# Kernel tuning notes

Measured on AMD Instinct MI355X. Metric: run time of the kernel, lower is better.

The kernel has to match this reference:

```python
import jax, jax.numpy as jnp
import numpy as np

KS = 3  # kernel_size
N, C_IN, C_OUT, H, W = 8, 64, 128, 256, 256


def _grid_sample_bilinear(img, gx, gy):
    """img [C,H,W]; gx, gy [Ho,Wo] normalized coords; align_corners=False, zero padding."""
    C, H_, W_ = img.shape
    ix = ((gx + 1.0) * W_ - 1.0) / 2.0
    iy = ((gy + 1.0) * H_ - 1.0) / 2.0
    x0 = jnp.floor(ix); y0 = jnp.floor(iy)
    x1 = x0 + 1.0;      y1 = y0 + 1.0
    wx1 = ix - x0; wx0 = 1.0 - wx1
    wy1 = iy - y0; wy0 = 1.0 - wy1

    def gather(yi, xi):
        valid = (xi >= 0) & (xi < W_) & (yi >= 0) & (yi < H_)
        xc = jnp.clip(xi, 0, W_ - 1).astype(jnp.int32)
        yc = jnp.clip(yi, 0, H_ - 1).astype(jnp.int32)
        v = img[:, yc, xc]  # [C,Ho,Wo]
        return v * valid[None].astype(img.dtype)

    out = (gather(y0, x0) * (wy0 * wx0)[None]
         + gather(y0, x1) * (wy0 * wx1)[None]
         + gather(y1, x0) * (wy1 * wx0)[None]
         + gather(y1, x1) * (wy1 * wx1)[None])
    return out


def setup_inputs() -> dict:
    key = jax.random.key(0)
    k1, k2, k3 = jax.random.split(key, 3)
    x = jax.random.normal(k1, (N, C_IN, H, W), dtype=jnp.float32)
    # offset conv: Conv2d(inc, 2*ks, ks, padding=(ks-1)//2, bias=False)
    offset_w = jax.random.normal(k2, (2 * KS, C_IN, KS, KS), dtype=jnp.float32) * 0.05
    # conv_kernel: Conv2d(inc, outc, kernel=(ks,1), stride=(ks,1), bias=False), kaiming fan_out
    fan_out = C_OUT * KS * 1
    conv_w = jax.random.normal(k3, (C_OUT, C_IN, KS, 1), dtype=jnp.float32) * np.sqrt(2.0 / fan_out)
    return {"x": x, "offset_w": offset_w, "conv_w": conv_w}


def reference(x, offset_w, conv_w):
    n, c, h, w = x.shape
    ks = KS
    pad = (ks - 1) // 2
    dn = ('NCHW', 'OIHW', 'NCHW')

    off = jax.lax.conv_general_dilated(x, offset_w, (1, 1), ((pad, pad), (pad, pad)),
                                       dimension_numbers=dn)  # [n,2ks,h,w]
    off = jnp.tanh(off).reshape(n, 2, ks, h, w)
    offset_y = off[:, 0]  # [n,ks,h,w]; x offsets are computed but unused in the original

    yc = (ks - 1) // 2
    # cumulative offsets radiating outward from the center row
    upper = jnp.cumsum(offset_y[:, yc:], axis=1)                       # indices yc..ks-1
    lower = jnp.cumsum(offset_y[:, :yc + 1][:, ::-1], axis=1)[:, ::-1]  # indices 0..yc
    y_new = jnp.concatenate([lower[:, :yc], upper], axis=1)            # [n,ks,h,w]

    # base grid replicates torch's repeat-then-reshape layout exactly:
    # flat pattern [-1,0,1,-1,0,1,...] of length ks*h*w, reshaped to (ks,h,w)
    vals = jnp.arange(-(ks - 1) // 2, (ks - 1) // 2 + 1, dtype=x.dtype)
    base = vals[jnp.arange(ks * h * w) % ks].reshape(ks, h, w)

    grid_y = (base[None] + y_new).reshape(n, ks * h, w)
    gy = grid_y / ((h - 1.0) / 2.0) - 1.0
    gx = jnp.full_like(gy, -1.0)  # grid_x is zeros -> 0/((w-1)/2) - 1 = -1

    sampled = jax.vmap(_grid_sample_bilinear)(x, gx, gy)  # [n,c,ks*h,w]

    out = jax.lax.conv_general_dilated(sampled, conv_w, (ks, 1), ((0, 0), (0, 0)),
                                       dimension_numbers=dn)  # [n,outc,h,w]
    return out
```

## Files before the change

kernel.cpp:

```cpp
#include <hip/hip_runtime.h>
#include <math.h>

#define H 256
#define W 256
#define NB 8
#define CIN 64
#define COUT 128
#define HW (H * W)

typedef float f4v __attribute__((ext_vector_type(4)));

__global__ __launch_bounds__(256) void kfused(const float* __restrict__ x,
                                              const float* __restrict__ offw,
                                              const float* __restrict__ convw,
                                              float* __restrict__ ynew,
                                              float* __restrict__ P) {
    if (blockIdx.z == NB) {
        __shared__ float xl[CIN * 4];
        __shared__ float wl[16 * 192];
        const int n = blockIdx.y;
        const int co0 = blockIdx.x * 16;
        const int tid = threadIdx.x;
        {
            int ci = tid >> 2, y = tid & 3;
            xl[tid] = x[(((size_t)n * CIN + ci) * H + y) * W];
        }
        for (int p = tid; p < 16 * 192; p += 256) wl[p] = convw[co0 * 192 + p];
        __syncthreads();
        if (tid < 192) {
            int co = tid / 12, t = tid - co * 12;
            int r = t >> 2, y = t & 3;
            float s = 0.f;
#pragma unroll
            for (int ci = 0; ci < CIN; ++ci) s += wl[co * 192 + ci * 3 + r] * xl[ci * 4 + y];
            P[((size_t)n * COUT + co0 + co) * 16 + t] = s;
        }
        return;
    }

    const int n = blockIdx.z;
    const int i0 = blockIdx.y * 32;
    const int j0 = blockIdx.x * 32;
    const int tid = threadIdx.x;
    const int wv = tid >> 6;
    const int lane = tid & 63;
    const int rloc = lane >> 3;
    const int q = lane & 7;
    const int orow = i0 + 8 * wv + rloc;
    const int jq = j0 + q * 4;
    const int lprev = (lane - 1) & 63;
    const int lnext = (lane + 1) & 63;

    const bool isq0 = (q == 0), isq7 = (q == 7);
    const int ecol = isq0 ? (j0 - 1) : (j0 + 32);
    const bool ecv = (isq0 | isq7) && ((unsigned)ecol < (unsigned)W);
    const int ecc = ecol < 0 ? 0 : (ecol > W - 1 ? W - 1 : ecol);

    const bool rv0 = (orow >= 1);
    const bool rv2 = (orow <= H - 2);
    const size_t ro0 = (size_t)(rv0 ? orow - 1 : 0) * W;
    const size_t ro1 = (size_t)orow * W;
    const size_t ro2 = (size_t)(rv2 ? orow + 1 : H - 1) * W;
    const bool ev0 = rv0 && ecv, ev1 = ecv, ev2 = rv2 && ecv;

    const float* xn = x + (size_t)n * CIN * HW;
    const float4 zf4 = make_float4(0.f, 0.f, 0.f, 0.f);

    float acc[3][4];
#pragma unroll
    for (int k = 0; k < 3; ++k)
#pragma unroll
        for (int d = 0; d < 4; ++d) acc[k][d] = 0.f;

#define LOADCH(c, M0, M1, M2, E0, E1, E2)                          \
    {                                                              \
        const float* xc = xn + (size_t)(c) * HW;                   \
        M0 = rv0 ? *(const float4*)(xc + ro0 + jq) : zf4;          \
        M1 = *(const float4*)(xc + ro1 + jq);                      \
        M2 = rv2 ? *(const float4*)(xc + ro2 + jq) : zf4;          \
        E0 = ev0 ? xc[ro0 + ecc] : 0.f;                            \
        E1 = ev1 ? xc[ro1 + ecc] : 0.f;                            \
        E2 = ev2 ? xc[ro2 + ecc] : 0.f;                            \
    }

#define CU(u, M, E)                                                \
    {                                                              \
        float lf = __shfl(M.w, lprev);                             \
        float rt = __shfl(M.x, lnext);                             \
        if (isq0) lf = E;                                          \
        if (isq7) rt = E;                                          \
        const float r0 = lf, r1 = M.x, r2 = M.y, r3 = M.z,         \
                    r4 = M.w, r5 = rt;                             \
        _Pragma("unroll") for (int k = 0; k < 3; ++k) {            \
            const float w0 = wp[k * 576 + (u)*3 + 0];              \
            const float w1 = wp[k * 576 + (u)*3 + 1];              \
            const float w2 = wp[k * 576 + (u)*3 + 2];              \
            acc[k][0] += r0 * w0 + r1 * w1 + r2 * w2;              \
            acc[k][1] += r1 * w0 + r2 * w1 + r3 * w2;              \
            acc[k][2] += r2 * w0 + r3 * w1 + r4 * w2;              \
            acc[k][3] += r3 * w0 + r4 * w1 + r5 * w2;              \
        }                                                          \
    }

#define COMPUTE(c, M0, M1, M2, E0, E1, E2)                         \
    {                                                              \
        const float* wp = offw + (size_t)(c) * 9;                  \
        CU(0, M0, E0) CU(1, M1, E1) CU(2, M2, E2)                  \
    }

    float4 Am0, Am1, Am2, Bm0, Bm1, Bm2;
    float Ae0, Ae1, Ae2, Be0, Be1, Be2;
    LOADCH(0, Am0, Am1, Am2, Ae0, Ae1, Ae2);
    LOADCH(1, Bm0, Bm1, Bm2, Be0, Be1, Be2);

    for (int c = 0; c < CIN; c += 2) {
        COMPUTE(c, Am0, Am1, Am2, Ae0, Ae1, Ae2);
        if (c + 2 < CIN) LOADCH(c + 2, Am0, Am1, Am2, Ae0, Ae1, Ae2);
        COMPUTE(c + 1, Bm0, Bm1, Bm2, Be0, Be1, Be2);
        if (c + 3 < CIN) LOADCH(c + 3, Bm0, Bm1, Bm2, Be0, Be1, Be2);
    }
#undef LOADCH
#undef CU
#undef COMPUTE

    float y[3][4];
#pragma unroll
    for (int d = 0; d < 4; ++d) {
        float t0 = tanhf(acc[0][d]);
        float t1 = tanhf(acc[1][d]);
        float t2 = tanhf(acc[2][d]);
        y[0][d] = t0 + t1;
        y[1][d] = t1;
        y[2][d] = t1 + t2;
    }
    size_t base = (size_t)n * 3 * HW + (size_t)orow * W + jq;
#pragma unroll
    for (int k = 0; k < 3; ++k)
        *(float4*)(ynew + base + (size_t)k * HW) =
            make_float4(y[k][0], y[k][1], y[k][2], y[k][3]);
}

__global__ __launch_bounds__(256) void kout(const float* __restrict__ ynew,
                                            const float* __restrict__ P,
                                            float* __restrict__ out) {
    __shared__ float Cs[12 * 256];
    __shared__ float Pl[128 * 16];
    const int n = blockIdx.y;
    const int i = blockIdx.x;
    const int tid = threadIdx.x;

    {
        const f4v* src = (const f4v*)(P + (size_t)n * COUT * 16);
        f4v* dst = (f4v*)Pl;
        dst[tid] = src[tid];
        dst[tid + 256] = src[tid + 256];
    }

    {
        const int j = tid;
        float c[12];
#pragma unroll
        for (int t = 0; t < 12; ++t) c[t] = 0.f;
#pragma unroll
        for (int r = 0; r < 3; ++r) {
            int rowi = 3 * i + r;
            int k = rowi >> 8;
            int i2 = rowi & 255;
            float g = (float)(((k + i2 + j) % 3) - 1) +
                      ynew[((size_t)n * 3 + k) * (H * W) + i2 * W + j];
            float gy = g / 127.5f - 1.0f;
            float iy = ((gy + 1.0f) * 256.0f - 1.0f) * 0.5f;
            float fy = floorf(iy);
            int y0 = (int)fy;
            float w1 = iy - fy;
            if ((unsigned)y0 < 4u) c[r * 4 + y0] += 0.5f * (1.0f - w1);
            int y1 = y0 + 1;
            if ((unsigned)y1 < 4u) c[r * 4 + y1] += 0.5f * w1;
        }
#pragma unroll
        for (int t = 0; t < 12; ++t) Cs[t * 256 + j] = c[t];
    }
    __syncthreads();

    const int jq = (tid & 63) * 4;
    const int cg = tid >> 6;
    float4 cc[12];
#pragma unroll
    for (int t = 0; t < 12; ++t) cc[t] = *(const float4*)&Cs[t * 256 + jq];

    float* op = out + (((size_t)n * COUT) * H + i) * W;
    for (int co = cg * 32; co < cg * 32 + 32; ++co) {
        const float4* pp = (const float4*)&Pl[co * 16];
        float4 P0 = pp[0], P1 = pp[1], P2 = pp[2];
        float pv[12] = {P0.x, P0.y, P0.z, P0.w, P1.x, P1.y, P1.z, P1.w,
                        P2.x, P2.y, P2.z, P2.w};
        f4v a = {0.f, 0.f, 0.f, 0.f};
#pragma unroll
        for (int t = 0; t < 12; ++t) {
            a.x += pv[t] * cc[t].x;
            a.y += pv[t] * cc[t].y;
            a.z += pv[t] * cc[t].z;
            a.w += pv[t] * cc[t].w;
        }
        __builtin_nontemporal_store(a, (f4v*)(op + (size_t)co * (H * W) + jq));
    }
}

extern "C" void kernel_launch(void* const* d_in, const int* in_sizes, int n_in,
                              void* d_out, int out_size, void* d_ws, size_t ws_size,
                              hipStream_t stream) {
    const float* x = (const float*)d_in[0];
    const float* offw = (const float*)d_in[1];
    const float* convw = (const float*)d_in[2];
    float* out = (float*)d_out;

    float* ynew = (float*)d_ws;
    float* P = ynew + (size_t)NB * 3 * HW;

    kfused<<<dim3(8, 8, NB + 1), 256, 0, stream>>>(x, offw, convw, ynew, P);
    kout<<<dim3(H, NB), 256, 0, stream>>>(ynew, P, out);
}
```

Before: 422.1 us.

## Split offset-conv channels across waves with per-wave LDS tiles and register rows

```diff
diff --git a/kernel.cpp b/kernel.cpp
--- a/kernel.cpp
+++ b/kernel.cpp
@@ -7,17 +7,23 @@
 #define CIN 64
 #define COUT 128
 #define HW (H * W)
+#define TROWS 34
+#define TCOLS 40
+#define TFLOATS (TROWS * TCOLS)
+#define TF4 (TFLOATS / 4)
 
 typedef float f4v __attribute__((ext_vector_type(4)));
 
-__global__ __launch_bounds__(256) void kfused(const float* __restrict__ x,
-                                              const float* __restrict__ offw,
-                                              const float* __restrict__ convw,
-                                              float* __restrict__ ynew,
-                                              float* __restrict__ P) {
+__global__ __launch_bounds__(256, 2) void kfused(const float* __restrict__ x,
+                                                 const float* __restrict__ offw,
+                                                 const float* __restrict__ convw,
+                                                 float* __restrict__ ynew,
+                                                 float* __restrict__ P) {
+    __shared__ float smem[12288];
+
     if (blockIdx.z == NB) {
-        __shared__ float xl[CIN * 4];
-        __shared__ float wl[16 * 192];
+        float* xl = smem;
+        float* wl = smem + 256;
         const int n = blockIdx.y;
         const int co0 = blockIdx.x * 16;
         const int tid = threadIdx.x;
@@ -44,100 +50,129 @@
     const int tid = threadIdx.x;
     const int wv = tid >> 6;
     const int lane = tid & 63;
-    const int rloc = lane >> 3;
+    const int rg = lane >> 3;
     const int q = lane & 7;
-    const int orow = i0 + 8 * wv + rloc;
-    const int jq = j0 + q * 4;
-    const int lprev = (lane - 1) & 63;
-    const int lnext = (lane + 1) & 63;
-
-    const bool isq0 = (q == 0), isq7 = (q == 7);
-    const int ecol = isq0 ? (j0 - 1) : (j0 + 32);
-    const bool ecv = (isq0 | isq7) && ((unsigned)ecol < (unsigned)W);
-    const int ecc = ecol < 0 ? 0 : (ecol > W - 1 ? W - 1 : ecol);
-
-    const bool rv0 = (orow >= 1);
-    const bool rv2 = (orow <= H - 2);
-    const size_t ro0 = (size_t)(rv0 ? orow - 1 : 0) * W;
-    const size_t ro1 = (size_t)orow * W;
-    const size_t ro2 = (size_t)(rv2 ? orow + 1 : H - 1) * W;
-    const bool ev0 = rv0 && ecv, ev1 = ecv, ev2 = rv2 && ecv;
-
-    const float* xn = x + (size_t)n * CIN * HW;
+
+    float* t0 = smem + wv * (2 * TFLOATS);
+    float* t1 = t0 + TFLOATS;
+
+    int offs[6];
+    bool vms[6];
+#pragma unroll
+    for (int m = 0; m < 6; ++m) {
+        int s = lane + (m << 6);
+        int a = s / 10, c4 = s - a * 10;
+        int gi = i0 - 1 + a;
+        int gj = j0 - 4 + (c4 << 2);
+        bool v = (s < TF4) && ((unsigned)gi < (unsigned)H) && ((unsigned)gj < (unsigned)W);
+        vms[m] = v;
+        offs[m] = v ? (gi * W + gj) : 0;
+    }
+
     const float4 zf4 = make_float4(0.f, 0.f, 0.f, 0.f);
-
-    float acc[3][4];
-#pragma unroll
-    for (int k = 0; k < 3; ++k)
-#pragma unroll
-        for (int d = 0; d < 4; ++d) acc[k][d] = 0.f;
-
-#define LOADCH(c, M0, M1, M2, E0, E1, E2)                          \
-    {                                                              \
-        const float* xc = xn + (size_t)(c) * HW;                   \
-        M0 = rv0 ? *(const float4*)(xc + ro0 + jq) : zf4;          \
-        M1 = *(const float4*)(xc + ro1 + jq);                      \
-        M2 = rv2 ? *(const float4*)(xc + ro2 + jq) : zf4;          \
-        E0 = ev0 ? xc[ro0 + ecc] : 0.f;                            \
-        E1 = ev1 ? xc[ro1 + ecc] : 0.f;                            \
-        E2 = ev2 ? xc[ro2 + ecc] : 0.f;                            \
-    }
-
-#define CU(u, M, E)                                                \
-    {                                                              \
-        float lf = __shfl(M.w, lprev);                             \
-        float rt = __shfl(M.x, lnext);                             \
-        if (isq0) lf = E;                                          \
-        if (isq7) rt = E;                                          \
-        const float r0 = lf, r1 = M.x, r2 = M.y, r3 = M.z,         \
-                    r4 = M.w, r5 = rt;                             \
-        _Pragma("unroll") for (int k = 0; k < 3; ++k) {            \
-            const float w0 = wp[k * 576 + (u)*3 + 0];              \
-            const float w1 = wp[k * 576 + (u)*3 + 1];              \
-            const float w2 = wp[k * 576 + (u)*3 + 2];              \
-            acc[k][0] += r0 * w0 + r1 * w1 + r2 * w2;              \
-            acc[k][1] += r1 * w0 + r2 * w1 + r3 * w2;              \
-            acc[k][2] += r2 * w0 + r3 * w1 + r4 * w2;              \
-            acc[k][3] += r3 * w0 + r4 * w1 + r5 * w2;              \
-        }                                                          \
-    }
-
-#define COMPUTE(c, M0, M1, M2, E0, E1, E2)                         \
-    {                                                              \
-        const float* wp = offw + (size_t)(c) * 9;                  \
-        CU(0, M0, E0) CU(1, M1, E1) CU(2, M2, E2)                  \
-    }
-
-    float4 Am0, Am1, Am2, Bm0, Bm1, Bm2;
-    float Ae0, Ae1, Ae2, Be0, Be1, Be2;
-    LOADCH(0, Am0, Am1, Am2, Ae0, Ae1, Ae2);
-    LOADCH(1, Bm0, Bm1, Bm2, Be0, Be1, Be2);
-
-    for (int c = 0; c < CIN; c += 2) {
-        COMPUTE(c, Am0, Am1, Am2, Ae0, Ae1, Ae2);
-        if (c + 2 < CIN) LOADCH(c + 2, Am0, Am1, Am2, Ae0, Ae1, Ae2);
-        COMPUTE(c + 1, Bm0, Bm1, Bm2, Be0, Be1, Be2);
-        if (c + 3 < CIN) LOADCH(c + 3, Bm0, Bm1, Bm2, Be0, Be1, Be2);
-    }
-#undef LOADCH
-#undef CU
-#undef COMPUTE
-
-    float y[3][4];
+    float acc[4][3][4];
+#pragma unroll
+    for (int ri = 0; ri < 4; ++ri)
+#pragma unroll
+        for (int k = 0; k < 3; ++k)
+#pragma unroll
+            for (int d = 0; d < 4; ++d) acc[ri][k][d] = 0.f;
+
+#define LOADC(cptr, R)                                                      \
+    _Pragma("unroll") for (int m = 0; m < 6; ++m)                           \
+        R[m] = vms[m] ? *(const float4*)((cptr) + offs[m]) : zf4;
+
+#define STAGE(buf, R)                                                       \
+    _Pragma("unroll") for (int m = 0; m < 6; ++m)                           \
+        if (m < 5 || lane < (TF4 - 320))                                    \
+            *(float4*)((buf) + ((lane + (m << 6)) << 2)) = R[m];
+
+#define COMPCH(buf, wp)                                                     \
+    {                                                                       \
+        _Pragma("unroll") for (int t = 0; t < 6; ++t) {                     \
+            const float* rp = (buf) + (4 * rg + t) * TCOLS + 4 * q;         \
+            float4 b0 = *(const float4*)(rp);                               \
+            float4 b1 = *(const float4*)(rp + 4);                           \
+            float4 b2 = *(const float4*)(rp + 8);                           \
+            const float r0 = b0.w, r1 = b1.x, r2 = b1.y, r3 = b1.z,         \
+                        r4 = b1.w, r5 = b2.x;                               \
+            _Pragma("unroll") for (int ri = 0; ri < 4; ++ri) {              \
+                if (ri < ((t - 2 > 0) ? t - 2 : 0) || ri > ((t < 3) ? t : 3)) continue; \
+                const int u = t - ri;                                       \
+                _Pragma("unroll") for (int k = 0; k < 3; ++k) {             \
+                    const float w0 = (wp)[k * 576 + u * 3 + 0];             \
+                    const float w1 = (wp)[k * 576 + u * 3 + 1];             \
+                    const float w2 = (wp)[k * 576 + u * 3 + 2];             \
+                    acc[ri][k][0] += r0 * w0 + r1 * w1 + r2 * w2;           \
+                    acc[ri][k][1] += r1 * w0 + r2 * w1 + r3 * w2;           \
+                    acc[ri][k][2] += r2 * w0 + r3 * w1 + r4 * w2;           \
+                    acc[ri][k][3] += r3 * w0 + r4 * w1 + r5 * w2;           \
+                }                                                           \
+            }                                                               \
+        }                                                                   \
+    }
+
+    const int c0 = wv << 4;
+    const float* xw = x + ((size_t)n * CIN + c0) * HW;
+    const float* wp0 = offw + (size_t)c0 * 9;
+
+    float4 RA[6], RB[6];
+    LOADC(xw, RA);
+    LOADC(xw + HW, RB);
+
+    for (int cc = 0; cc < 16; cc += 2) {
+        STAGE(t0, RA);
+        if (cc + 2 < 16) {
+            const float* xp = xw + (size_t)(cc + 2) * HW;
+            LOADC(xp, RA);
+        }
+        COMPCH(t0, wp0 + (size_t)cc * 9);
+        STAGE(t1, RB);
+        if (cc + 3 < 16) {
+            const float* xp = xw + (size_t)(cc + 3) * HW;
+            LOADC(xp, RB);
+        }
+        COMPCH(t1, wp0 + (size_t)(cc + 1) * 9);
+    }
+#undef LOADC
+#undef STAGE
+#undef COMPCH
+
+    __syncthreads();
+#pragma unroll
+    for (int ri = 0; ri < 4; ++ri)
+#pragma unroll
+        for (int k = 0; k < 3; ++k)
+#pragma unroll
+            for (int d = 0; d < 4; ++d)
+                smem[((wv * 48 + ri * 12 + k * 4 + d) << 6) + lane] = acc[ri][k][d];
+    __syncthreads();
+
+    const int row = tid >> 3;
+    const int q2 = tid & 7;
+    const int srcl = ((row >> 2) << 3) | q2;
+    const int rbase = (row & 3) * 12;
+
+    float y0[4], y1[4], y2[4];
 #pragma unroll
     for (int d = 0; d < 4; ++d) {
-        float t0 = tanhf(acc[0][d]);
-        float t1 = tanhf(acc[1][d]);
-        float t2 = tanhf(acc[2][d]);
-        y[0][d] = t0 + t1;
-        y[1][d] = t1;
-        y[2][d] = t1 + t2;
-    }
-    size_t base = (size_t)n * 3 * HW + (size_t)orow * W + jq;
-#pragma unroll
-    for (int k = 0; k < 3; ++k)
-        *(float4*)(ynew + base + (size_t)k * HW) =
-            make_float4(y[k][0], y[k][1], y[k][2], y[k][3]);
+        float s0 = 0.f, s1 = 0.f, s2 = 0.f;
+#pragma unroll
+        for (int w = 0; w < 4; ++w) {
+            const float* bp = smem + ((w * 48 + rbase) << 6) + srcl;
+            s0 += bp[(0 * 4 + d) << 6];
+            s1 += bp[(1 * 4 + d) << 6];
+            s2 += bp[(2 * 4 + d) << 6];
+        }
+        float v0 = tanhf(s0), v1 = tanhf(s1), v2 = tanhf(s2);
+        y0[d] = v0 + v1;
+        y1[d] = v1;
+        y2[d] = v1 + v2;
+    }
+    size_t base = (size_t)n * 3 * HW + (size_t)(i0 + row) * W + (j0 + (q2 << 2));
+    *(float4*)(ynew + base) = make_float4(y0[0], y0[1], y0[2], y0[3]);
+    *(float4*)(ynew + base + (size_t)HW) = make_float4(y1[0], y1[1], y1[2], y1[3]);
+    *(float4*)(ynew + base + (size_t)2 * HW) = make_float4(y2[0], y2[1], y2[2], y2[3]);
 }
 
 __global__ __launch_bounds__(256) void kout(const float* __restrict__ ynew,
```

Result: slower. 453.3 us (+7.4%).
